# Kernel tuning notes

Measured on AMD Instinct MI355X. Metric: run time of the kernel, lower is better.

## Reference

```python
import jax, jax.numpy as jnp
import numpy as np

N = 1_000_000
C = 32
DIMS = (480, 360, 32)  # cylindrical voxel grid (z/rho, phi, height)
EPS = 1e-5


def setup_inputs() -> dict:
    rng = np.random.default_rng(0)
    total = DIMS[0] * DIMS[1] * DIMS[2]
    # unique active voxels, sorted so searchsorted gives row indices directly
    ids = np.sort(rng.choice(total, size=N, replace=False)).astype(np.int64)
    z = ids // (DIMS[1] * DIMS[2])
    rem = ids % (DIMS[1] * DIMS[2])
    y = rem // DIMS[2]
    x = rem % DIMS[2]
    coords = np.stack([z, y, x], axis=1)
    strides = np.array([DIMS[1] * DIMS[2], DIMS[2], 1], dtype=np.int64)

    def nbr(delta):
        out = np.full((3, N), -1, dtype=np.int32)
        for a in range(3):
            tgt = ids + delta * strides[a]
            ok = (coords[:, a] + delta >= 0) & (coords[:, a] + delta < DIMS[a])
            pos = np.searchsorted(ids, tgt)
            pos_c = np.clip(pos, 0, N - 1)
            found = ok & (ids[pos_c] == tgt)
            out[a] = np.where(found, pos_c, -1).astype(np.int32)
        return out

    nbr_prev = nbr(-1)
    nbr_next = nbr(+1)

    key = jax.random.key(0)
    k0, k1, k2 = jax.random.split(key, 3)
    features = jax.random.normal(k0, (N, C), dtype=jnp.float32)
    # W[branch, tap, in, out]; taps ordered (-1, 0, +1) along the branch's axis
    W = jax.random.normal(k1, (3, 3, C, C), dtype=jnp.float32) * (1.0 / np.sqrt(3 * C))
    gamma = jnp.ones((3, C), dtype=jnp.float32)
    beta = jnp.zeros((3, C), dtype=jnp.float32)
    mean = jax.random.normal(k2, (3, C), dtype=jnp.float32) * 0.1
    var = jnp.ones((3, C), dtype=jnp.float32)
    return {
        "features": features,
        "nbr_prev": jnp.asarray(nbr_prev),
        "nbr_next": jnp.asarray(nbr_next),
        "W": W,
        "gamma": gamma,
        "beta": beta,
        "mean": mean,
        "var": var,
    }


def _branch(f, Wb, prev, nxt, g, b, m, v):
    # 3-tap submanifold conv along one axis: gather prev/next active neighbors
    pm = prev >= 0
    nm = nxt >= 0
    fp = jnp.where(pm[:, None], f[jnp.where(pm, prev, 0)], 0.0)
    fn = jnp.where(nm[:, None], f[jnp.where(nm, nxt, 0)], 0.0)
    out = fp @ Wb[0] + f @ Wb[1] + fn @ Wb[2]
    # BatchNorm1d (inference stats) + Sigmoid
    out = (out - m) * (g * jax.lax.rsqrt(v + EPS)) + b
    return jax.nn.sigmoid(out)


def reference(features, nbr_prev, nbr_next, W, gamma, beta, mean, var):
    acc = jnp.zeros_like(features)
    for a in range(3):  # conv3x1x1, conv1x3x1, conv1x1x3
        acc = acc + _branch(features, W[a], nbr_prev[a], nbr_next[a],
                            gamma[a], beta[a], mean[a], var[a])
    return acc * features  # sparse_add then gating with input features
```

## Files before the change

### kernel.cpp

```cpp
#include <hip/hip_runtime.h>
#include <stdint.h>


typedef __attribute__((ext_vector_type(8))) __bf16 bf16x8;
typedef __attribute__((ext_vector_type(8))) unsigned short u16x8;
typedef __attribute__((ext_vector_type(4))) float f32x4;
typedef __attribute__((ext_vector_type(2))) float f32x2;

constexpr int NVOX    = 1000000;
constexpr int NTILES  = NVOX / 16;
constexpr int TPW     = 2;
constexpr int WPB     = 4;
constexpr int NWAVES  = (NTILES + TPW - 1) / TPW;
constexpr int NBLOCKS = (NWAVES + WPB - 1) / WPB;
constexpr float LOG2E = 1.4426950408889634f;

constexpr int WS_WELEMS = 18 * 64 * 8;

__global__ __launch_bounds__(256) void prep_kernel(
    const float* __restrict__ Wt,
    const float* __restrict__ gma, const float* __restrict__ bta,
    const float* __restrict__ mea, const float* __restrict__ var,
    unsigned short* __restrict__ wsW, float* __restrict__ wsA,
    float* __restrict__ wsB)
{
    int tid = blockIdx.x * 256 + threadIdx.x;
    if (tid < WS_WELEMS) {
        int f    = tid >> 9;
        int rem  = tid & 511;
        int lane = rem >> 3;
        int j    = rem & 7;
        int br = f / 6, t = (f >> 1) % 3, h = f & 1;
        int n = lane & 15, quad = lane >> 4;
        float w = Wt[((br * 3 + t) * 32 + quad * 8 + j) * 32 + 2 * n + h];
        union { float f; unsigned u; } c; c.f = w;
        wsW[(f * 64 + lane) * 8 + j] = (unsigned short)((c.u + 0x8000u) >> 16);
    } else if (tid < WS_WELEMS + 96) {
        int i = tid - WS_WELEMS;
        float s = gma[i] * __frsqrt_rn(var[i] + 1e-5f);
        wsA[i] = -s * LOG2E;
        wsB[i] = (mea[i] * s - bta[i]) * LOG2E;
    }
}

__device__ __forceinline__ unsigned pack_bf(float a, float b) {
    union { float f; unsigned u; } ca, cb; ca.f = a; cb.f = b;
    return __builtin_amdgcn_perm(cb.u + 0x8000u, ca.u + 0x8000u, 0x07060302u);
}
__device__ __forceinline__ bf16x8 cvt_frag(f32x4 lo, f32x4 hi) {
    union { unsigned u[4]; bf16x8 v; } r;
    r.u[0] = pack_bf(lo[0], lo[1]); r.u[1] = pack_bf(lo[2], lo[3]);
    r.u[2] = pack_bf(hi[0], hi[1]); r.u[3] = pack_bf(hi[2], hi[3]);
    return r.v;
}

__global__ __launch_bounds__(256) void recon_kernel(
    const float*          __restrict__ feat,
    const int*            __restrict__ nprev,
    const int*            __restrict__ nnext,
    const unsigned short* __restrict__ wsW,
    const float*          __restrict__ wsA,
    const float*          __restrict__ wsB,
    float*                __restrict__ out)
{
    const int lane = threadIdx.x & 63;
    const int n    = lane & 15;
    const int quad = lane >> 4;

    int b   = blockIdx.x;
    int per = NBLOCKS / 8;
    int bs  = (b < per * 8) ? ((b & 7) * per + (b >> 3)) : b;
    int wv  = bs * WPB + (threadIdx.x >> 6);

    const int t0 = wv * TPW;
    if (t0 >= NTILES) return;

    bf16x8 Bf[18];
    #pragma unroll
    for (int f = 0; f < 18; ++f)
        Bf[f] = __builtin_bit_cast(bf16x8, *(const u16x8*)(wsW + (f * 64 + lane) * 8));

    f32x2 A_[3], B_[3];
    #pragma unroll
    for (int br = 0; br < 3; ++br) {
        A_[br] = *(const f32x2*)(wsA + br * 32 + 2 * n);
        B_[br] = *(const f32x2*)(wsB + br * 32 + 2 * n);
    }

    int ip[3], inx[3];
    {
        int row0 = t0 * 16 + n;
        #pragma unroll
        for (int a = 0; a < 3; ++a) {
            ip[a]  = nprev[a * NVOX + row0];
            inx[a] = nnext[a * NVOX + row0];
        }
    }

    #pragma unroll 1
    for (int tt = 0; tt < TPW; ++tt) {
        int tile = t0 + tt;
        if (tile >= NTILES) break;
        int base = tile * 16;
        int row  = base + n;

        const f32x4* ps = (const f32x4*)(feat + row * 32 + quad * 8);
        f32x4 s_lo = ps[0], s_hi = ps[1];
        f32x4 p_lo[3], p_hi[3], n_lo[3], n_hi[3];
        #pragma unroll
        for (int a = 0; a < 3; ++a) {
            p_lo[a] = (f32x4){0.f, 0.f, 0.f, 0.f}; p_hi[a] = p_lo[a];
            n_lo[a] = p_lo[a];                     n_hi[a] = p_lo[a];
            if (ip[a] >= 0) {
                const f32x4* pp = (const f32x4*)(feat + ip[a] * 32 + quad * 8);
                p_lo[a] = pp[0]; p_hi[a] = pp[1];
            }
            if (inx[a] >= 0) {
                const f32x4* pn = (const f32x4*)(feat + inx[a] * 32 + quad * 8);
                n_lo[a] = pn[0]; n_hi[a] = pn[1];
            }
        }

        int ipn[3], inn[3];
        if (tt + 1 < TPW && tile + 1 < NTILES) {
            int nrow = row + 16;
            #pragma unroll
            for (int a = 0; a < 3; ++a) {
                ipn[a] = nprev[a * NVOX + nrow];
                inn[a] = nnext[a * NVOX + nrow];
            }
        } else {
            #pragma unroll
            for (int a = 0; a < 3; ++a) { ipn[a] = -1; inn[a] = -1; }
        }

        bf16x8 Aself = cvt_frag(s_lo, s_hi);
        bf16x8 Ap[3], An[3];
        #pragma unroll
        for (int a = 0; a < 3; ++a) {
            Ap[a] = cvt_frag(p_lo[a], p_hi[a]);
            An[a] = cvt_frag(n_lo[a], n_hi[a]);
        }

        f32x4 acc0 = {0.f, 0.f, 0.f, 0.f}, acc1 = {0.f, 0.f, 0.f, 0.f};
        #pragma unroll
        for (int br = 0; br < 3; ++br) {
            f32x4 c0 = {0.f, 0.f, 0.f, 0.f}, c1 = {0.f, 0.f, 0.f, 0.f};
            c0 = __builtin_amdgcn_mfma_f32_16x16x32_bf16(Ap[br], Bf[br*6 + 0], c0, 0, 0, 0);
            c1 = __builtin_amdgcn_mfma_f32_16x16x32_bf16(Ap[br], Bf[br*6 + 1], c1, 0, 0, 0);
            c0 = __builtin_amdgcn_mfma_f32_16x16x32_bf16(Aself,  Bf[br*6 + 2], c0, 0, 0, 0);
            c1 = __builtin_amdgcn_mfma_f32_16x16x32_bf16(Aself,  Bf[br*6 + 3], c1, 0, 0, 0);
            c0 = __builtin_amdgcn_mfma_f32_16x16x32_bf16(An[br], Bf[br*6 + 4], c0, 0, 0, 0);
            c1 = __builtin_amdgcn_mfma_f32_16x16x32_bf16(An[br], Bf[br*6 + 5], c1, 0, 0, 0);
            float a0 = A_[br][0], b0 = B_[br][0], a1 = A_[br][1], b1 = B_[br][1];
            #pragma unroll
            for (int r = 0; r < 4; ++r) {
                float e0 = __builtin_amdgcn_exp2f(__builtin_fmaf(c0[r], a0, b0));
                float e1 = __builtin_amdgcn_exp2f(__builtin_fmaf(c1[r], a1, b1));
                acc0[r] += __builtin_amdgcn_rcpf(1.0f + e0);
                acc1[r] += __builtin_amdgcn_rcpf(1.0f + e1);
            }
        }

        #pragma unroll
        for (int r = 0; r < 4; ++r) {
            int vrow = base + quad * 4 + r;
            f32x2 fv = *(const f32x2*)(feat + vrow * 32 + 2 * n);
            f32x2 ov = { acc0[r] * fv[0], acc1[r] * fv[1] };
            *(f32x2*)(out + vrow * 32 + 2 * n) = ov;
        }

        #pragma unroll
        for (int a = 0; a < 3; ++a) { ip[a] = ipn[a]; inx[a] = inn[a]; }
    }
}

extern "C" void kernel_launch(void* const* d_in, const int* in_sizes, int n_in,
                              void* d_out, int out_size, void* d_ws, size_t ws_size,
                              hipStream_t stream) {
    const float* feat  = (const float*)d_in[0];
    const int*   nprev = (const int*)d_in[1];
    const int*   nnext = (const int*)d_in[2];
    const float* Wt    = (const float*)d_in[3];
    const float* gma   = (const float*)d_in[4];
    const float* bta   = (const float*)d_in[5];
    const float* mea   = (const float*)d_in[6];
    const float* var   = (const float*)d_in[7];
    float*       o     = (float*)d_out;

    unsigned short* wsW = (unsigned short*)d_ws;
    float*          wsA = (float*)((char*)d_ws + WS_WELEMS * 2);
    float*          wsB = wsA + 96;

    prep_kernel<<<(WS_WELEMS + 96 + 255) / 256, 256, 0, stream>>>(
        Wt, gma, bta, mea, var, wsW, wsA, wsB);
    recon_kernel<<<NBLOCKS, 256, 0, stream>>>(feat, nprev, nnext,
                                              wsW, wsA, wsB, o);
}
```

Baseline: 317.5 us.

## Pre-convert features to bf16 and gather neighbors from compact bf16 copy

Adds a pass that converts the fp32 feature matrix into a bf16 copy in workspace. The main kernel then gathers the seven neighbor rows per voxel from that copy, so each random gather moves half the bytes. Missing neighbors read a zeroed dummy row, which removes the branches. Weights are staged in LDS instead of registers, each wave handles four tiles with double-buffered gathers, and the output stores are nontemporal. The cost is an extra full read and write of the features, plus a fallback path for when the workspace is too small.

Measured after the change: 304.8 us. 1.04x faster.

```diff
diff --git a/kernel.cpp b/kernel.cpp
--- a/kernel.cpp
+++ b/kernel.cpp
@@ -9,20 +9,28 @@
 
 constexpr int NVOX    = 1000000;
 constexpr int NTILES  = NVOX / 16;
-constexpr int TPW     = 2;
 constexpr int WPB     = 4;
-constexpr int NWAVES  = (NTILES + TPW - 1) / TPW;
-constexpr int NBLOCKS = (NWAVES + WPB - 1) / WPB;
 constexpr float LOG2E = 1.4426950408889634f;
 
-constexpr int WS_WELEMS = 18 * 64 * 8;
+constexpr int TPW4     = 4;
+constexpr int NWAVES4  = NTILES / TPW4;
+constexpr int NBLOCKS4 = (NWAVES4 + WPB - 1) / WPB;
+
+constexpr int TPW2     = 2;
+constexpr int NWAVES2  = (NTILES + TPW2 - 1) / TPW2;
+constexpr int NBLOCKS2 = (NWAVES2 + WPB - 1) / WPB;
+
+constexpr int    WS_WELEMS = 18 * 64 * 8;
+constexpr size_t FB_BYTES  = (size_t)NVOX * 64;
+constexpr unsigned ZOFF    = (unsigned)(FB_BYTES + 18432 + 768);
+constexpr size_t WS_NEED   = FB_BYTES + 18432 + 768 + 128;
 
 __global__ __launch_bounds__(256) void prep_kernel(
     const float* __restrict__ Wt,
     const float* __restrict__ gma, const float* __restrict__ bta,
     const float* __restrict__ mea, const float* __restrict__ var,
     unsigned short* __restrict__ wsW, float* __restrict__ wsA,
-    float* __restrict__ wsB)
+    float* __restrict__ wsB, float* __restrict__ wsZ)
 {
     int tid = blockIdx.x * 256 + threadIdx.x;
     if (tid < WS_WELEMS) {
@@ -40,6 +48,8 @@
         float s = gma[i] * __frsqrt_rn(var[i] + 1e-5f);
         wsA[i] = -s * LOG2E;
         wsB[i] = (mea[i] * s - bta[i]) * LOG2E;
+    } else if (wsZ != nullptr && tid < WS_WELEMS + 96 + 32) {
+        wsZ[tid - WS_WELEMS - 96] = 0.0f;
     }
 }
 
@@ -54,7 +64,163 @@
     return r.v;
 }
 
-__global__ __launch_bounds__(256) void recon_kernel(
+__global__ __launch_bounds__(256) void cvt_feat(
+    const float* __restrict__ f, unsigned short* __restrict__ fb)
+{
+    int tid = blockIdx.x * 256 + threadIdx.x;
+    const f32x4* p = (const f32x4*)(f + (size_t)tid * 8);
+    f32x4 lo = p[0], hi = p[1];
+    union { unsigned u[4]; u16x8 v; } r;
+    r.u[0] = pack_bf(lo[0], lo[1]); r.u[1] = pack_bf(lo[2], lo[3]);
+    r.u[2] = pack_bf(hi[0], hi[1]); r.u[3] = pack_bf(hi[2], hi[3]);
+    *(u16x8*)(fb + (size_t)tid * 8) = r.v;
+}
+
+__device__ __forceinline__ f32x4 mfma16(u16x8 a, bf16x8 b, f32x4 c) {
+    return __builtin_amdgcn_mfma_f32_16x16x32_bf16(
+        __builtin_bit_cast(bf16x8, a), b, c, 0, 0, 0);
+}
+
+__global__ __launch_bounds__(256) void recon_bf16(
+    const float* __restrict__ feat,
+    const int*   __restrict__ nprev,
+    const int*   __restrict__ nnext,
+    const char*  __restrict__ fbc,
+    const unsigned short* __restrict__ wsW,
+    const float* __restrict__ wsA,
+    const float* __restrict__ wsB,
+    float*       __restrict__ out)
+{
+    __shared__ unsigned short smem[WS_WELEMS];
+    {
+        const u16x8* s = (const u16x8*)wsW;
+        u16x8* d = (u16x8*)smem;
+        #pragma unroll
+        for (int i = 0; i < 5; ++i) {
+            int k = (int)threadIdx.x + i * 256;
+            if (k < 18 * 64) d[k] = s[k];
+        }
+    }
+    __syncthreads();
+
+    const int lane = threadIdx.x & 63;
+    const int n    = lane & 15;
+    const int quad = lane >> 4;
+    const unsigned qo = (unsigned)quad * 16u;
+
+    int b   = blockIdx.x;
+    int per = NBLOCKS4 / 8;
+    int bs  = (b < per * 8) ? ((b & 7) * per + (b >> 3)) : b;
+    int wv  = bs * WPB + (threadIdx.x >> 6);
+    if (wv >= NWAVES4) return;
+    const int t0 = wv * TPW4;
+
+    f32x2 A_[3], B_[3];
+    #pragma unroll
+    for (int br = 0; br < 3; ++br) {
+        A_[br] = *(const f32x2*)(wsA + br * 32 + 2 * n);
+        B_[br] = *(const f32x2*)(wsB + br * 32 + 2 * n);
+    }
+
+    unsigned lbase = (unsigned)lane * 16u;
+
+    int idxP[2][3], idxN[2][3];
+    {
+        int r0 = t0 * 16 + n;
+        #pragma unroll
+        for (int a = 0; a < 3; ++a) {
+            idxP[0][a] = nprev[a * NVOX + r0];
+            idxN[0][a] = nnext[a * NVOX + r0];
+            idxP[1][a] = nprev[a * NVOX + r0 + 16];
+            idxN[1][a] = nnext[a * NVOX + r0 + 16];
+        }
+    }
+
+    u16x8 G[2][7];
+    {
+        int row0 = t0 * 16 + n;
+        G[0][0] = *(const u16x8*)(fbc + (unsigned)row0 * 64u + qo);
+        #pragma unroll
+        for (int a = 0; a < 3; ++a) {
+            unsigned op = idxP[0][a] >= 0 ? (unsigned)idxP[0][a] * 64u : ZOFF;
+            unsigned on = idxN[0][a] >= 0 ? (unsigned)idxN[0][a] * 64u : ZOFF;
+            G[0][1 + a] = *(const u16x8*)(fbc + op + qo);
+            G[0][4 + a] = *(const u16x8*)(fbc + on + qo);
+        }
+    }
+
+    #pragma unroll
+    for (int tt = 0; tt < TPW4; ++tt) {
+        const int cur  = tt & 1;
+        const int nxt  = cur ^ 1;
+        const int base = (t0 + tt) * 16;
+
+        f32x2 fv[4];
+        #pragma unroll
+        for (int r = 0; r < 4; ++r)
+            fv[r] = __builtin_nontemporal_load(
+                (const f32x2*)(feat + (base + quad * 4 + r) * 32 + 2 * n));
+
+        if (tt + 1 < TPW4) {
+            int rown = base + 16 + n;
+            G[nxt][0] = *(const u16x8*)(fbc + (unsigned)rown * 64u + qo);
+            #pragma unroll
+            for (int a = 0; a < 3; ++a) {
+                unsigned op = idxP[nxt][a] >= 0 ? (unsigned)idxP[nxt][a] * 64u : ZOFF;
+                unsigned on = idxN[nxt][a] >= 0 ? (unsigned)idxN[nxt][a] * 64u : ZOFF;
+                G[nxt][1 + a] = *(const u16x8*)(fbc + op + qo);
+                G[nxt][4 + a] = *(const u16x8*)(fbc + on + qo);
+            }
+        }
+        if (tt + 2 < TPW4) {
+            int r2 = base + 32 + n;
+            #pragma unroll
+            for (int a = 0; a < 3; ++a) {
+                idxP[cur][a] = nprev[a * NVOX + r2];
+                idxN[cur][a] = nnext[a * NVOX + r2];
+            }
+        }
+
+        asm volatile("" : "+v"(lbase));
+        const char* sb = (const char*)smem + lbase;
+
+        f32x4 acc0 = {0.f, 0.f, 0.f, 0.f}, acc1 = {0.f, 0.f, 0.f, 0.f};
+        #pragma unroll
+        for (int br = 0; br < 3; ++br) {
+            bf16x8 w0 = *(const bf16x8*)(sb + (br * 6 + 0) * 1024);
+            bf16x8 w1 = *(const bf16x8*)(sb + (br * 6 + 1) * 1024);
+            bf16x8 w2 = *(const bf16x8*)(sb + (br * 6 + 2) * 1024);
+            bf16x8 w3 = *(const bf16x8*)(sb + (br * 6 + 3) * 1024);
+            bf16x8 w4 = *(const bf16x8*)(sb + (br * 6 + 4) * 1024);
+            bf16x8 w5 = *(const bf16x8*)(sb + (br * 6 + 5) * 1024);
+            f32x4 c0 = {0.f, 0.f, 0.f, 0.f}, c1 = {0.f, 0.f, 0.f, 0.f};
+            c0 = mfma16(G[cur][1 + br], w0, c0);
+            c1 = mfma16(G[cur][1 + br], w1, c1);
+            c0 = mfma16(G[cur][0],      w2, c0);
+            c1 = mfma16(G[cur][0],      w3, c1);
+            c0 = mfma16(G[cur][4 + br], w4, c0);
+            c1 = mfma16(G[cur][4 + br], w5, c1);
+            float a0 = A_[br][0], b0 = B_[br][0];
+            float a1 = A_[br][1], b1 = B_[br][1];
+            #pragma unroll
+            for (int r = 0; r < 4; ++r) {
+                float e0 = __builtin_amdgcn_exp2f(__builtin_fmaf(c0[r], a0, b0));
+                float e1 = __builtin_amdgcn_exp2f(__builtin_fmaf(c1[r], a1, b1));
+                acc0[r] += __builtin_amdgcn_rcpf(1.0f + e0);
+                acc1[r] += __builtin_amdgcn_rcpf(1.0f + e1);
+            }
+        }
+
+        #pragma unroll
+        for (int r = 0; r < 4; ++r) {
+            int vrow = base + quad * 4 + r;
+            f32x2 ov = { acc0[r] * fv[r][0], acc1[r] * fv[r][1] };
+            __builtin_nontemporal_store(ov, (f32x2*)(out + vrow * 32 + 2 * n));
+        }
+    }
+}
+
+__global__ __launch_bounds__(256) void recon_legacy(
     const float*          __restrict__ feat,
     const int*            __restrict__ nprev,
     const int*            __restrict__ nnext,
@@ -68,11 +234,11 @@
     const int quad = lane >> 4;
 
     int b   = blockIdx.x;
-    int per = NBLOCKS / 8;
+    int per = NBLOCKS2 / 8;
     int bs  = (b < per * 8) ? ((b & 7) * per + (b >> 3)) : b;
     int wv  = bs * WPB + (threadIdx.x >> 6);
 
-    const int t0 = wv * TPW;
+    const int t0 = wv * TPW2;
     if (t0 >= NTILES) return;
 
     bf16x8 Bf[18];
@@ -98,7 +264,7 @@
     }
 
     #pragma unroll 1
-    for (int tt = 0; tt < TPW; ++tt) {
+    for (int tt = 0; tt < TPW2; ++tt) {
         int tile = t0 + tt;
         if (tile >= NTILES) break;
         int base = tile * 16;
@@ -122,7 +288,7 @@
         }
 
         int ipn[3], inn[3];
-        if (tt + 1 < TPW && tile + 1 < NTILES) {
+        if (tt + 1 < TPW2 && tile + 1 < NTILES) {
             int nrow = row + 16;
             #pragma unroll
             for (int a = 0; a < 3; ++a) {
@@ -188,12 +354,24 @@
     const float* var   = (const float*)d_in[7];
     float*       o     = (float*)d_out;
 
-    unsigned short* wsW = (unsigned short*)d_ws;
-    float*          wsA = (float*)((char*)d_ws + WS_WELEMS * 2);
-    float*          wsB = wsA + 96;
-
-    prep_kernel<<<(WS_WELEMS + 96 + 255) / 256, 256, 0, stream>>>(
-        Wt, gma, bta, mea, var, wsW, wsA, wsB);
-    recon_kernel<<<NBLOCKS, 256, 0, stream>>>(feat, nprev, nnext,
-                                              wsW, wsA, wsB, o);
-}
+    if (ws_size >= WS_NEED) {
+        unsigned short* fb  = (unsigned short*)d_ws;
+        unsigned short* wsW = (unsigned short*)((char*)d_ws + FB_BYTES);
+        float* wsA = (float*)((char*)d_ws + FB_BYTES + 18432);
+        float* wsB = wsA + 96;
+        float* wsZ = wsB + 96;
+        prep_kernel<<<(WS_WELEMS + 96 + 32 + 255) / 256, 256, 0, stream>>>(
+            Wt, gma, bta, mea, var, wsW, wsA, wsB, wsZ);
+        cvt_feat<<<(NVOX * 32) / (256 * 8), 256, 0, stream>>>(feat, fb);
+        recon_bf16<<<NBLOCKS4, 256, 0, stream>>>(feat, nprev, nnext,
+            (const char*)d_ws, wsW, wsA, wsB, o);
+    } else {
+        unsigned short* wsW = (unsigned short*)d_ws;
+        float* wsA = (float*)((char*)d_ws + WS_WELEMS * 2);
+        float* wsB = wsA + 96;
+        prep_kernel<<<(WS_WELEMS + 96 + 255) / 256, 256, 0, stream>>>(
+            Wt, gma, bta, mea, var, wsW, wsA, wsB, nullptr);
+        recon_legacy<<<NBLOCKS2, 256, 0, stream>>>(feat, nprev, nnext,
+                                                   wsW, wsA, wsB, o);
+    }
+}
```
